# Kernel optimization log

Hardware: AMD Instinct MI355X
Metric: run time of the kernel (lower is better)

## Reference

```python
import jax, jax.numpy as jnp
import numpy as np

D_MODEL = 1024
N_HEADS = 16
D_HEAD = D_MODEL // N_HEADS
ROPE_BASE = 10000.0
EPS = float(jnp.finfo(jnp.float32).eps)  # torch RMSNorm default eps


def _rmsnorm(x, g):
    # x: (..., d_head), g: (d_head,)
    var = jnp.mean(x * x, axis=-1, keepdims=True)
    return x * jax.lax.rsqrt(var + EPS) * g


def _rope(x, pos):
    # x: (B, H, L, d), pos: (L,) int
    d = x.shape[-1]
    inv_freq = 1.0 / (ROPE_BASE ** (jnp.arange(0, d, 2, dtype=jnp.float32) / d))  # (d/2,)
    ang = pos.astype(jnp.float32)[:, None] * inv_freq[None, :]                    # (L, d/2)
    cos, sin = jnp.cos(ang), jnp.sin(ang)                                         # (L, d/2)
    x1, x2 = jnp.split(x, 2, axis=-1)
    return jnp.concatenate([x1 * cos - x2 * sin, x1 * sin + x2 * cos], axis=-1)


def setup_inputs() -> dict:
    key = jax.random.key(0)
    ks = jax.random.split(key, 6)
    B, Lq, Lk = 4, 2048, 2048
    s = 0.02
    return {
        "queries": jax.random.normal(ks[0], (B, Lq, D_MODEL), dtype=jnp.float32),
        "kv": jax.random.normal(ks[1], (B, Lk, D_MODEL), dtype=jnp.float32),
        "Wq": jax.random.normal(ks[2], (D_MODEL, D_MODEL), dtype=jnp.float32) * s,
        "Wkv": jax.random.normal(ks[3], (D_MODEL, 2 * D_MODEL), dtype=jnp.float32) * s,
        "Wout": jax.random.normal(ks[4], (D_MODEL, D_MODEL), dtype=jnp.float32) * s,
        "g_q": jnp.ones((D_HEAD,), dtype=jnp.float32),
        "g_k": jnp.ones((D_HEAD,), dtype=jnp.float32),
        "pos_q": jnp.arange(Lq, dtype=jnp.int64 if jax.config.jax_enable_x64 else jnp.int32),
        "pos_k": jnp.arange(Lk, dtype=jnp.int64 if jax.config.jax_enable_x64 else jnp.int32),
    }


def reference(queries, kv, Wq, Wkv, Wout, g_q, g_k, pos_q, pos_k):
    B, Lq, D = queries.shape
    Lk = kv.shape[1]
    H, d = N_HEADS, D_HEAD
    # projections (bias=False)
    q = (queries @ Wq).reshape(B, Lq, H, d).transpose(0, 2, 1, 3)          # (B,H,Lq,d)
    kvp = (kv @ Wkv).reshape(B, Lk, H, 2 * d).transpose(0, 2, 1, 3)        # (B,H,Lk,2d)
    k, v = kvp[..., :d], kvp[..., d:]
    # per-head RMSNorm on q/k
    q = _rmsnorm(q, g_q)
    k = _rmsnorm(k, g_k)
    # RoPE
    q = _rope(q, pos_q)
    k = _rope(k, pos_k)
    # attention (non-causal, no mask, no dropout)
    scale = d ** -0.5
    scores = jnp.einsum("bhqd,bhkd->bhqk", q, k) * scale                   # (B,H,Lq,Lk)
    attn = jax.nn.softmax(scores, axis=-1)
    y = jnp.einsum("bhqk,bhkd->bhqd", attn, v)                             # (B,H,Lq,d)
    y = y.transpose(0, 2, 1, 3).reshape(B, Lq, D)
    return y @ Wout
```

## Files before the change

kernel.cpp:

```cpp
#include <hip/hip_runtime.h>

#define DEVI __device__ __forceinline__

typedef __bf16 bf16;
typedef __attribute__((ext_vector_type(8))) __bf16 bf16x8v;
typedef __attribute__((ext_vector_type(4))) __bf16 bf16x4v;
typedef __attribute__((ext_vector_type(16))) float f32x16;

constexpr int LKV = 2048;

DEVI void gload16(const void* g, void* l) {
  __builtin_amdgcn_global_load_lds((__attribute__((address_space(1))) void*)g,
                                   (__attribute__((address_space(3))) void*)l, 16, 0, 0);
}

DEVI bf16x8v ldfrag(const bf16* base, int row, int clog) {
  int cphys = clog ^ (row & 7);
  return *(const bf16x8v*)(base + row * 64 + cphys * 8);
}

DEVI unsigned pk2(float a, float b) {
  unsigned short ha = __builtin_bit_cast(unsigned short, (__bf16)a);
  unsigned short hb = __builtin_bit_cast(unsigned short, (__bf16)b);
  return (unsigned)ha | ((unsigned)hb << 16);
}

__global__ void cast_bf16_kernel(const float* __restrict__ in, bf16* __restrict__ out, int n8) {
  int i = blockIdx.x * blockDim.x + threadIdx.x;
  if (i >= n8) return;
  long base = (long)i * 8;
  float4 a = *(const float4*)(in + base);
  float4 b = *(const float4*)(in + base + 4);
  bf16x8v v;
  v[0] = (bf16)a.x; v[1] = (bf16)a.y; v[2] = (bf16)a.z; v[3] = (bf16)a.w;
  v[4] = (bf16)b.x; v[5] = (bf16)b.y; v[6] = (bf16)b.z; v[7] = (bf16)b.w;
  *(bf16x8v*)(out + base) = v;
}

__global__ void wtrans_kernel(const float* __restrict__ W, bf16* __restrict__ Wt, int K, int N) {
  __shared__ float t[32][33];
  int n0 = blockIdx.x * 32, k0 = blockIdx.y * 32;
  int tx = threadIdx.x, ty = threadIdx.y;
  #pragma unroll
  for (int i = 0; i < 4; ++i) t[ty + i * 8][tx] = W[(long)(k0 + ty + i * 8) * N + n0 + tx];
  __syncthreads();
  #pragma unroll
  for (int i = 0; i < 4; ++i) Wt[(long)(n0 + ty + i * 8) * K + k0 + tx] = (bf16)t[tx][ty + i * 8];
}

template<bool OUT_BF16>
__global__ __launch_bounds__(256, 2)
void gemm_bf16_kernel(const bf16* __restrict__ A, const bf16* __restrict__ Bt,
                      void* __restrict__ C, int M, int N, int K, int NXB) {
  __shared__ bf16 As[128 * 64];
  __shared__ bf16 Bs[128 * 64];
  const int tid = threadIdx.x;
  const int wid = tid >> 6, lane = tid & 63;
  const int ln31 = lane & 31, hi = lane >> 5;
  const int wr = wid >> 1, wc = wid & 1;
  const int cpx = gridDim.x >> 3;
  const int wg = blockIdx.x;
  const int flat = (wg & 7) * cpx + (wg >> 3);
  const int by = flat / NXB, bx = flat - by * NXB;
  const int tM = by * 128, tN = bx * 128;
  f32x16 acc[2][2] = {};
  for (int kt = 0; kt < K; kt += 64) {
    #pragma unroll
    for (int p = 0; p < 8; ++p) {
      int cidx = p * 4 + wid;
      int row = (cidx & 15) * 8 + (lane >> 3);
      int clog = (lane & 7) ^ (row & 7);
      if (cidx < 16)
        gload16(A + (long)(tM + row) * K + kt + clog * 8, As + cidx * 512);
      else
        gload16(Bt + (long)(tN + row) * K + kt + clog * 8, Bs + (cidx - 16) * 512);
    }
    __syncthreads();
    #pragma unroll
    for (int st = 0; st < 4; ++st) {
      int clog = st * 2 + hi;
      bf16x8v a0 = ldfrag(As, wr * 64 + ln31, clog);
      bf16x8v a1 = ldfrag(As, wr * 64 + 32 + ln31, clog);
      bf16x8v b0 = ldfrag(Bs, wc * 64 + ln31, clog);
      bf16x8v b1 = ldfrag(Bs, wc * 64 + 32 + ln31, clog);
      acc[0][0] = __builtin_amdgcn_mfma_f32_32x32x16_bf16(a0, b0, acc[0][0], 0, 0, 0);
      acc[0][1] = __builtin_amdgcn_mfma_f32_32x32x16_bf16(a0, b1, acc[0][1], 0, 0, 0);
      acc[1][0] = __builtin_amdgcn_mfma_f32_32x32x16_bf16(a1, b0, acc[1][0], 0, 0, 0);
      acc[1][1] = __builtin_amdgcn_mfma_f32_32x32x16_bf16(a1, b1, acc[1][1], 0, 0, 0);
    }
    __syncthreads();
  }
  #pragma unroll
  for (int mi = 0; mi < 2; ++mi)
    #pragma unroll
    for (int ni = 0; ni < 2; ++ni)
      #pragma unroll
      for (int rr = 0; rr < 4; ++rr)
        #pragma unroll
        for (int j = 0; j < 4; ++j) {
          int mrow = tM + wr * 64 + mi * 32 + rr * 8 + hi * 4 + j;
          int ncol = tN + wc * 64 + ni * 32 + ln31;
          float v = acc[mi][ni][rr * 4 + j];
          if (OUT_BF16) ((bf16*)C)[(long)mrow * N + ncol] = (bf16)v;
          else          ((float*)C)[(long)mrow * N + ncol] = v;
        }
}

__global__ void rope_tab_kernel(const int* __restrict__ pos, float2* __restrict__ tab, float scale) {
  int idx = blockIdx.x * 256 + threadIdx.x;
  int l = idx >> 5, i = idx & 31;
  float ang = (float)pos[l] * __expf((float)i * -0.28782313662425575f);
  float sn, cs;
  sincosf(ang, &sn, &cs);
  tab[idx] = make_float2(cs * scale, sn * scale);
}

__global__ void rope_qk_kernel(const bf16* __restrict__ X, bf16* __restrict__ Out,
                               const float* __restrict__ g, const float2* __restrict__ tab,
                               int colStride, int colOff) {
  int tid = threadIdx.x; int wid = tid >> 6; int lane = tid & 63;
  long w = (long)blockIdx.x * 4 + wid;
  int h = (int)(w & 15); long bl = w >> 4;
  int l = (int)(bl & 2047); int b = (int)(bl >> 11);
  float x = (float)X[bl * colStride + h * colOff + lane];
  float ss = x * x;
  #pragma unroll
  for (int m = 32; m >= 1; m >>= 1) ss += __shfl_xor(ss, m);
  float rs = rsqrtf(ss * (1.0f / 64.0f) + 1.1920928955078125e-07f);
  x *= rs * g[lane];
  float other = __shfl_xor(x, 32);
  float2 cssn = tab[l * 32 + (lane & 31)];
  float y = x * cssn.x + ((lane < 32) ? -other : other) * cssn.y;
  int bh = b * 16 + h;
  Out[((long)bh * 2048 + l) * 64 + lane] = (bf16)y;
}

__global__ void transpose_v_kernel(const unsigned short* __restrict__ KVp, unsigned short* __restrict__ Vt) {
  __shared__ unsigned short t[64][65];
  int bh = blockIdx.y; int b = bh >> 4, h = bh & 15;
  long lt = (long)blockIdx.x * 64;
  int tid = threadIdx.x; int c = tid & 63; int r0 = tid >> 6;
  #pragma unroll
  for (int i = 0; i < 16; ++i) {
    int l = i * 4 + r0;
    t[l][c] = KVp[((long)(b * 2048) + lt + l) * 2048 + h * 128 + 64 + c];
  }
  __syncthreads();
  #pragma unroll
  for (int i = 0; i < 16; ++i) {
    int dv = i * 4 + r0;
    Vt[((long)(bh * 64 + dv)) * 2048 + lt + c] = t[c][dv];
  }
}

__global__ __launch_bounds__(256, 2)
void attn_kernel(const bf16* __restrict__ Q, const bf16* __restrict__ Kr,
                 const bf16* __restrict__ Vt, bf16* __restrict__ Y) {
  __shared__ bf16 Ks[2 * 4096];
  __shared__ bf16 Vs[2 * 4096];
  const int tid = threadIdx.x, wid = tid >> 6, lane = tid & 63;
  const int ln31 = lane & 31, hi = lane >> 5;
  const int wg = blockIdx.x;
  const int flat = (wg & 7) * 128 + (wg >> 3);
  const int bh = flat >> 4, qb = flat & 15;
  const int qg = qb * 128 + wid * 32 + ln31;

  const int rsub = lane >> 3, csub = lane & 7;
  int r0 = wid * 8 + rsub;        int s0 = csub ^ (r0 & 7);
  int r1 = (wid + 4) * 8 + rsub;  int s1 = csub ^ (r1 & 7);
  const bf16* gp0 = Kr + ((long)bh * 2048 + r0) * 64 + s0 * 8;
  const bf16* gp1 = Kr + ((long)bh * 2048 + r1) * 64 + s1 * 8;
  const bf16* gp2 = Vt + ((long)(bh * 64 + r0)) * 2048 + s0 * 8;
  const bf16* gp3 = Vt + ((long)(bh * 64 + r1)) * 2048 + s1 * 8;
  bf16* lk0 = Ks + wid * 512;
  bf16* lk1 = Ks + (wid + 4) * 512;
  bf16* lv0 = Vs + wid * 512;
  bf16* lv1 = Vs + (wid + 4) * 512;

  const bf16* Qrow = Q + ((long)bh * 2048 + qg) * 64;
  bf16x8v qf[4];
  #pragma unroll
  for (int st = 0; st < 4; ++st) qf[st] = *(const bf16x8v*)(Qrow + st * 16 + hi * 8);
  f32x16 o[2] = {};
  float srun = 0.0f;

  gload16(gp0, lk0); gp0 += 4096;
  gload16(gp1, lk1); gp1 += 4096;
  gload16(gp2, lv0); gp2 += 64;
  gload16(gp3, lv1); gp3 += 64;
  __syncthreads();

  int boff = 0;
  for (int kt = 0; kt < LKV; kt += 64) {
    if (kt + 64 < LKV) {
      int nb = boff ^ 4096;
      gload16(gp0, lk0 + nb); gp0 += 4096;
      gload16(gp1, lk1 + nb); gp1 += 4096;
      gload16(gp2, lv0 + nb); gp2 += 64;
      gload16(gp3, lv1 + nb); gp3 += 64;
    }
    const bf16* kb = Ks + boff;
    const bf16* vb = Vs + boff;

    f32x16 sT[2] = {};
    #pragma unroll
    for (int st = 0; st < 4; ++st) {
      int clog = st * 2 + hi;
      bf16x8v k0 = ldfrag(kb, ln31, clog);
      bf16x8v k1 = ldfrag(kb, 32 + ln31, clog);
      sT[0] = __builtin_amdgcn_mfma_f32_32x32x16_bf16(k0, qf[st], sT[0], 0, 0, 0);
      sT[1] = __builtin_amdgcn_mfma_f32_32x32x16_bf16(k1, qf[st], sT[1], 0, 0, 0);
    }

    float p0 = 0.0f, p1 = 0.0f, p2 = 0.0f, p3 = 0.0f;
    #pragma unroll
    for (int mf = 0; mf < 2; ++mf) {
      #pragma unroll
      for (int r = 0; r < 16; r += 4) {
        float e0 = __builtin_amdgcn_exp2f(sT[mf][r + 0]);
        float e1 = __builtin_amdgcn_exp2f(sT[mf][r + 1]);
        float e2 = __builtin_amdgcn_exp2f(sT[mf][r + 2]);
        float e3 = __builtin_amdgcn_exp2f(sT[mf][r + 3]);
        sT[mf][r + 0] = e0; sT[mf][r + 1] = e1; sT[mf][r + 2] = e2; sT[mf][r + 3] = e3;
        p0 += e0; p1 += e1; p2 += e2; p3 += e3;
      }
    }
    srun += (p0 + p1) + (p2 + p3);

    #pragma unroll
    for (int kb_ = 0; kb_ < 4; ++kb_) {
      int mf = kb_ >> 1; int rb = (kb_ & 1) * 8;
      unsigned w0 = pk2(sT[mf][rb + 0], sT[mf][rb + 1]);
      unsigned w1 = pk2(sT[mf][rb + 2], sT[mf][rb + 3]);
      unsigned w2 = pk2(sT[mf][rb + 4], sT[mf][rb + 5]);
      unsigned w3 = pk2(sT[mf][rb + 6], sT[mf][rb + 7]);
      asm("v_permlane32_swap_b32 %0, %1" : "+v"(w0), "+v"(w2));
      asm("v_permlane32_swap_b32 %0, %1" : "+v"(w1), "+v"(w3));
      uint4 uw = make_uint4(w0, w1, w2, w3);
      bf16x8v pf = __builtin_bit_cast(bf16x8v, uw);
      int clog = kb_ * 2 + hi;
      bf16x8v v0 = ldfrag(vb, ln31, clog);
      bf16x8v v1 = ldfrag(vb, 32 + ln31, clog);
      o[0] = __builtin_amdgcn_mfma_f32_32x32x16_bf16(v0, pf, o[0], 0, 0, 0);
      o[1] = __builtin_amdgcn_mfma_f32_32x32x16_bf16(v1, pf, o[1], 0, 0, 0);
    }
    __syncthreads();
    boff ^= 4096;
  }

  srun += __shfl_xor(srun, 32);
  float inv = 1.0f / srun;
  int b = bh >> 4, h = bh & 15;
  long orow = ((long)(b * 2048 + qg)) * 1024 + h * 64;
  #pragma unroll
  for (int mfo = 0; mfo < 2; ++mfo)
    #pragma unroll
    for (int rr = 0; rr < 4; ++rr) {
      bf16x4v wv;
      #pragma unroll
      for (int j = 0; j < 4; ++j) wv[j] = (bf16)(o[mfo][rr * 4 + j] * inv);
      *(bf16x4v*)(Y + orow + mfo * 32 + rr * 8 + hi * 4) = wv;
    }
}

extern "C" void kernel_launch(void* const* d_in, const int* in_sizes, int n_in,
                              void* d_out, int out_size, void* d_ws, size_t ws_size,
                              hipStream_t stream) {
  const float* queries = (const float*)d_in[0];
  const float* kv      = (const float*)d_in[1];
  const float* Wq      = (const float*)d_in[2];
  const float* Wkv     = (const float*)d_in[3];
  const float* Wout    = (const float*)d_in[4];
  const float* g_q     = (const float*)d_in[5];
  const float* g_k     = (const float*)d_in[6];
  const int*   pos_q   = (const int*)d_in[7];
  const int*   pos_k   = (const int*)d_in[8];

  char* ws = (char*)d_ws;
  bf16* Qb    = (bf16*)ws; ws += (long)8192 * 1024 * 2;
  bf16* KVb   = (bf16*)ws; ws += (long)8192 * 1024 * 2;
  bf16* Wqt   = (bf16*)ws; ws += (long)1024 * 1024 * 2;
  bf16* Wkvt  = (bf16*)ws; ws += (long)2048 * 1024 * 2;
  bf16* Woutt = (bf16*)ws; ws += (long)1024 * 1024 * 2;
  bf16* Qp    = (bf16*)ws; ws += (long)8192 * 1024 * 2;
  bf16* KVp   = (bf16*)ws; ws += (long)8192 * 2048 * 2;
  bf16* Qr    = (bf16*)ws; ws += (long)8192 * 1024 * 2;
  bf16* Kr    = (bf16*)ws; ws += (long)8192 * 1024 * 2;
  bf16* Vt    = (bf16*)ws; ws += (long)8192 * 1024 * 2;
  bf16* Y     = (bf16*)ws; ws += (long)8192 * 1024 * 2;
  float2* tabq = (float2*)ws; ws += (long)65536 * 8;
  float2* tabk = (float2*)ws; ws += (long)65536 * 8;

  rope_tab_kernel<<<256, 256, 0, stream>>>(pos_q, tabq, 0.18033688011112042f);
  rope_tab_kernel<<<256, 256, 0, stream>>>(pos_k, tabk, 1.0f);

  cast_bf16_kernel<<<4096, 256, 0, stream>>>(queries, Qb, 8192 * 1024 / 8);
  cast_bf16_kernel<<<4096, 256, 0, stream>>>(kv, KVb, 8192 * 1024 / 8);
  wtrans_kernel<<<dim3(32, 32), dim3(32, 8), 0, stream>>>(Wq, Wqt, 1024, 1024);
  wtrans_kernel<<<dim3(64, 32), dim3(32, 8), 0, stream>>>(Wkv, Wkvt, 1024, 2048);
  wtrans_kernel<<<dim3(32, 32), dim3(32, 8), 0, stream>>>(Wout, Woutt, 1024, 1024);

  gemm_bf16_kernel<true><<<512, 256, 0, stream>>>(Qb, Wqt, Qp, 8192, 1024, 1024, 8);
  gemm_bf16_kernel<true><<<1024, 256, 0, stream>>>(KVb, Wkvt, KVp, 8192, 2048, 1024, 16);

  rope_qk_kernel<<<32768, 256, 0, stream>>>(Qp, Qr, g_q, tabq, 1024, 64);
  rope_qk_kernel<<<32768, 256, 0, stream>>>(KVp, Kr, g_k, tabk, 2048, 128);
  transpose_v_kernel<<<dim3(32, 64), 256, 0, stream>>>((const unsigned short*)KVp, (unsigned short*)Vt);

  attn_kernel<<<1024, 256, 0, stream>>>(Qr, Kr, Vt, Y);

  gemm_bf16_kernel<false><<<512, 256, 0, stream>>>(Y, Woutt, d_out, 8192, 1024, 1024, 8);
}
```

Measured before the change: 367.2 us.

## Replace projection GEMMs with 4-stage LDS ring pipeline and merge small kernels

The projection GEMMs are replaced by a 512-thread kernel with 128x256 or 256x256 tiles and K-step 32. It keeps a 4-deep LDS ring of async global-to-LDS loads (three stages in flight), uses a new swizzle, and raises wave priority around the MFMA block. It also merges the rope-table, cast, weight-transpose and rope kernels into single launches each. The aim is to hide global load latency behind MFMA work, raise tile reuse, and cut launch count. In exchange, LDS use per block is larger and the vmcnt counts are tuned by hand, so wrong counts would break correctness.

```diff
diff --git a/kernel.cpp b/kernel.cpp
--- a/kernel.cpp
+++ b/kernel.cpp
@@ -19,15 +19,24 @@
   return *(const bf16x8v*)(base + row * 64 + cphys * 8);
 }
 
+DEVI bf16x8v ldfrag_r(const bf16* R, int row, int c) {
+  int line = row >> 2;
+  int phys = ((row & 3) * 4 + c) ^ (line & 15);
+  return *(const bf16x8v*)(R + line * 128 + phys * 8);
+}
+
 DEVI unsigned pk2(float a, float b) {
   unsigned short ha = __builtin_bit_cast(unsigned short, (__bf16)a);
   unsigned short hb = __builtin_bit_cast(unsigned short, (__bf16)b);
   return (unsigned)ha | ((unsigned)hb << 16);
 }
 
-__global__ void cast_bf16_kernel(const float* __restrict__ in, bf16* __restrict__ out, int n8) {
-  int i = blockIdx.x * blockDim.x + threadIdx.x;
-  if (i >= n8) return;
+__global__ void cast2_kernel(const float* __restrict__ q, const float* __restrict__ kvp,
+                             bf16* __restrict__ Qb, bf16* __restrict__ KVb) {
+  int i = blockIdx.x * 256 + threadIdx.x;
+  const float* in; bf16* out;
+  if (i < 1048576) { in = q; out = Qb; }
+  else             { in = kvp; out = KVb; i -= 1048576; }
   long base = (long)i * 8;
   float4 a = *(const float4*)(in + base);
   float4 b = *(const float4*)(in + base + 4);
@@ -37,77 +46,116 @@
   *(bf16x8v*)(out + base) = v;
 }
 
-__global__ void wtrans_kernel(const float* __restrict__ W, bf16* __restrict__ Wt, int K, int N) {
+__global__ void wtrans3_kernel(const float* __restrict__ Wq, const float* __restrict__ Wkv,
+                               const float* __restrict__ Wout,
+                               bf16* __restrict__ Wqt, bf16* __restrict__ Wkvt,
+                               bf16* __restrict__ Woutt) {
   __shared__ float t[32][33];
-  int n0 = blockIdx.x * 32, k0 = blockIdx.y * 32;
+  int x = blockIdx.x;
+  const float* W; bf16* Wt; int N; int xb;
+  if (x < 32)      { W = Wq;   Wt = Wqt;   N = 1024; xb = x; }
+  else if (x < 96) { W = Wkv;  Wt = Wkvt;  N = 2048; xb = x - 32; }
+  else             { W = Wout; Wt = Woutt; N = 1024; xb = x - 96; }
+  int n0 = xb * 32, k0 = blockIdx.y * 32;
   int tx = threadIdx.x, ty = threadIdx.y;
   #pragma unroll
   for (int i = 0; i < 4; ++i) t[ty + i * 8][tx] = W[(long)(k0 + ty + i * 8) * N + n0 + tx];
   __syncthreads();
   #pragma unroll
-  for (int i = 0; i < 4; ++i) Wt[(long)(n0 + ty + i * 8) * K + k0 + tx] = (bf16)t[tx][ty + i * 8];
-}
-
-template<bool OUT_BF16>
-__global__ __launch_bounds__(256, 2)
-void gemm_bf16_kernel(const bf16* __restrict__ A, const bf16* __restrict__ Bt,
+  for (int i = 0; i < 4; ++i) Wt[(long)(n0 + ty + i * 8) * 1024 + k0 + tx] = (bf16)t[tx][ty + i * 8];
+}
+
+template<int BM, bool OUT_BF16>
+__global__ __launch_bounds__(512, 2)
+void gemm_ring_kernel(const bf16* __restrict__ A, const bf16* __restrict__ Bt,
                       void* __restrict__ C, int M, int N, int K, int NXB) {
-  __shared__ bf16 As[128 * 64];
-  __shared__ bf16 Bs[128 * 64];
+  constexpr int ROWS = BM + 256;
+  constexpr int REG  = ROWS * 32;
+  constexpr int NCH  = ROWS * 4;
+  constexpr int LPT  = NCH / 512;
+  constexpr int MI   = BM / 64;
+  __shared__ bf16 Lds[4 * REG];
   const int tid = threadIdx.x;
   const int wid = tid >> 6, lane = tid & 63;
   const int ln31 = lane & 31, hi = lane >> 5;
-  const int wr = wid >> 1, wc = wid & 1;
+  const int wm = wid >> 2, wn = wid & 3;
   const int cpx = gridDim.x >> 3;
   const int wg = blockIdx.x;
   const int flat = (wg & 7) * cpx + (wg >> 3);
   const int by = flat / NXB, bx = flat - by * NXB;
-  const int tM = by * 128, tN = bx * 128;
-  f32x16 acc[2][2] = {};
-  for (int kt = 0; kt < K; kt += 64) {
-    #pragma unroll
-    for (int p = 0; p < 8; ++p) {
-      int cidx = p * 4 + wid;
-      int row = (cidx & 15) * 8 + (lane >> 3);
-      int clog = (lane & 7) ^ (row & 7);
-      if (cidx < 16)
-        gload16(A + (long)(tM + row) * K + kt + clog * 8, As + cidx * 512);
-      else
-        gload16(Bt + (long)(tN + row) * K + kt + clog * 8, Bs + (cidx - 16) * 512);
-    }
-    __syncthreads();
-    #pragma unroll
-    for (int st = 0; st < 4; ++st) {
-      int clog = st * 2 + hi;
-      bf16x8v a0 = ldfrag(As, wr * 64 + ln31, clog);
-      bf16x8v a1 = ldfrag(As, wr * 64 + 32 + ln31, clog);
-      bf16x8v b0 = ldfrag(Bs, wc * 64 + ln31, clog);
-      bf16x8v b1 = ldfrag(Bs, wc * 64 + 32 + ln31, clog);
-      acc[0][0] = __builtin_amdgcn_mfma_f32_32x32x16_bf16(a0, b0, acc[0][0], 0, 0, 0);
-      acc[0][1] = __builtin_amdgcn_mfma_f32_32x32x16_bf16(a0, b1, acc[0][1], 0, 0, 0);
-      acc[1][0] = __builtin_amdgcn_mfma_f32_32x32x16_bf16(a1, b0, acc[1][0], 0, 0, 0);
-      acc[1][1] = __builtin_amdgcn_mfma_f32_32x32x16_bf16(a1, b1, acc[1][1], 0, 0, 0);
-    }
-    __syncthreads();
+  const long tM = (long)by * BM, tN = (long)bx * 256;
+  const int NS = K >> 5;
+
+  auto stage = [&](int s) {
+    bf16* region = Lds + (s & 3) * REG;
+    int kcol = s * 32;
+    #pragma unroll
+    for (int q = 0; q < LPT; ++q) {
+      int ci = q * 512 + tid;
+      int line = ci >> 4, phys = ci & 15;
+      int t = phys ^ (line & 15);
+      int row = line * 4 + (t >> 2), c = t & 3;
+      const bf16* src = (row < BM)
+        ? A  + (tM + row) * (long)K + kcol + c * 8
+        : Bt + (tN + row - BM) * (long)K + kcol + c * 8;
+      gload16(src, region + ci * 8);
+    }
+  };
+
+  f32x16 acc[MI][2] = {};
+  stage(0); stage(1); stage(2);
+
+  for (int s = 0; s < NS; ++s) {
+    if constexpr (LPT == 4) asm volatile("s_waitcnt vmcnt(8)" ::: "memory");
+    else                    asm volatile("s_waitcnt vmcnt(6)" ::: "memory");
+    __builtin_amdgcn_s_barrier();
+    __builtin_amdgcn_sched_barrier(0);
+    stage(s + 3);
+    const bf16* R = Lds + (s & 3) * REG;
+    bf16x8v a[MI][2], b[2][2];
+    #pragma unroll
+    for (int mi = 0; mi < MI; ++mi)
+      #pragma unroll
+      for (int ks = 0; ks < 2; ++ks)
+        a[mi][ks] = ldfrag_r(R, wm * (BM / 2) + mi * 32 + ln31, ks * 2 + hi);
+    #pragma unroll
+    for (int ni = 0; ni < 2; ++ni)
+      #pragma unroll
+      for (int ks = 0; ks < 2; ++ks)
+        b[ni][ks] = ldfrag_r(R, BM + wn * 64 + ni * 32 + ln31, ks * 2 + hi);
+    __builtin_amdgcn_s_setprio(1);
+    #pragma unroll
+    for (int ks = 0; ks < 2; ++ks)
+      #pragma unroll
+      for (int mi = 0; mi < MI; ++mi)
+        #pragma unroll
+        for (int ni = 0; ni < 2; ++ni)
+          acc[mi][ni] = __builtin_amdgcn_mfma_f32_32x32x16_bf16(a[mi][ks], b[ni][ks], acc[mi][ni], 0, 0, 0);
+    __builtin_amdgcn_s_setprio(0);
   }
-  #pragma unroll
-  for (int mi = 0; mi < 2; ++mi)
+
+  #pragma unroll
+  for (int mi = 0; mi < MI; ++mi)
     #pragma unroll
     for (int ni = 0; ni < 2; ++ni)
       #pragma unroll
       for (int rr = 0; rr < 4; ++rr)
         #pragma unroll
         for (int j = 0; j < 4; ++j) {
-          int mrow = tM + wr * 64 + mi * 32 + rr * 8 + hi * 4 + j;
-          int ncol = tN + wc * 64 + ni * 32 + ln31;
+          long mrow = tM + wm * (BM / 2) + mi * 32 + rr * 8 + hi * 4 + j;
+          long ncol = tN + wn * 64 + ni * 32 + ln31;
           float v = acc[mi][ni][rr * 4 + j];
-          if (OUT_BF16) ((bf16*)C)[(long)mrow * N + ncol] = (bf16)v;
-          else          ((float*)C)[(long)mrow * N + ncol] = v;
+          if (OUT_BF16) ((bf16*)C)[mrow * N + ncol] = (bf16)v;
+          else          ((float*)C)[mrow * N + ncol] = v;
         }
 }
 
-__global__ void rope_tab_kernel(const int* __restrict__ pos, float2* __restrict__ tab, float scale) {
+__global__ void rope_tab2_kernel(const int* __restrict__ pos_q, const int* __restrict__ pos_k,
+                                 float2* __restrict__ tabq, float2* __restrict__ tabk) {
   int idx = blockIdx.x * 256 + threadIdx.x;
+  const int* pos; float2* tab; float scale;
+  if (idx < 65536) { pos = pos_q; tab = tabq; scale = 0.18033688011112042f; }
+  else             { pos = pos_k; tab = tabk; scale = 1.0f; idx -= 65536; }
   int l = idx >> 5, i = idx & 31;
   float ang = (float)pos[l] * __expf((float)i * -0.28782313662425575f);
   float sn, cs;
@@ -115,11 +163,20 @@
   tab[idx] = make_float2(cs * scale, sn * scale);
 }
 
-__global__ void rope_qk_kernel(const bf16* __restrict__ X, bf16* __restrict__ Out,
-                               const float* __restrict__ g, const float2* __restrict__ tab,
-                               int colStride, int colOff) {
+__global__ void rope2_kernel(const bf16* __restrict__ Qp, const bf16* __restrict__ KVp,
+                             bf16* __restrict__ Qr, bf16* __restrict__ Kr,
+                             const float* __restrict__ g_q, const float* __restrict__ g_k,
+                             const float2* __restrict__ tabq, const float2* __restrict__ tabk) {
+  int bx = blockIdx.x;
+  bool isQ = bx < 32768;
+  int bb = isQ ? bx : bx - 32768;
+  const bf16* X = isQ ? Qp : KVp;
+  bf16* Out = isQ ? Qr : Kr;
+  const float* g = isQ ? g_q : g_k;
+  const float2* tab = isQ ? tabq : tabk;
+  int colStride = isQ ? 1024 : 2048, colOff = isQ ? 64 : 128;
   int tid = threadIdx.x; int wid = tid >> 6; int lane = tid & 63;
-  long w = (long)blockIdx.x * 4 + wid;
+  long w = (long)bb * 4 + wid;
   int h = (int)(w & 15); long bl = w >> 4;
   int l = (int)(bl & 2047); int b = (int)(bl >> 11);
   float x = (float)X[bl * colStride + h * colOff + lane];
@@ -291,23 +348,17 @@
   float2* tabq = (float2*)ws; ws += (long)65536 * 8;
   float2* tabk = (float2*)ws; ws += (long)65536 * 8;
 
-  rope_tab_kernel<<<256, 256, 0, stream>>>(pos_q, tabq, 0.18033688011112042f);
-  rope_tab_kernel<<<256, 256, 0, stream>>>(pos_k, tabk, 1.0f);
-
-  cast_bf16_kernel<<<4096, 256, 0, stream>>>(queries, Qb, 8192 * 1024 / 8);
-  cast_bf16_kernel<<<4096, 256, 0, stream>>>(kv, KVb, 8192 * 1024 / 8);
-  wtrans_kernel<<<dim3(32, 32), dim3(32, 8), 0, stream>>>(Wq, Wqt, 1024, 1024);
-  wtrans_kernel<<<dim3(64, 32), dim3(32, 8), 0, stream>>>(Wkv, Wkvt, 1024, 2048);
-  wtrans_kernel<<<dim3(32, 32), dim3(32, 8), 0, stream>>>(Wout, Woutt, 1024, 1024);
-
-  gemm_bf16_kernel<true><<<512, 256, 0, stream>>>(Qb, Wqt, Qp, 8192, 1024, 1024, 8);
-  gemm_bf16_kernel<true><<<1024, 256, 0, stream>>>(KVb, Wkvt, KVp, 8192, 2048, 1024, 16);
-
-  rope_qk_kernel<<<32768, 256, 0, stream>>>(Qp, Qr, g_q, tabq, 1024, 64);
-  rope_qk_kernel<<<32768, 256, 0, stream>>>(KVp, Kr, g_k, tabk, 2048, 128);
+  rope_tab2_kernel<<<512, 256, 0, stream>>>(pos_q, pos_k, tabq, tabk);
+  cast2_kernel<<<8192, 256, 0, stream>>>(queries, kv, Qb, KVb);
+  wtrans3_kernel<<<dim3(128, 32), dim3(32, 8), 0, stream>>>(Wq, Wkv, Wout, Wqt, Wkvt, Woutt);
+
+  gemm_ring_kernel<128, true><<<256, 512, 0, stream>>>(Qb, Wqt, Qp, 8192, 1024, 1024, 4);
+  gemm_ring_kernel<256, true><<<256, 512, 0, stream>>>(KVb, Wkvt, KVp, 8192, 2048, 1024, 8);
+
+  rope2_kernel<<<65536, 256, 0, stream>>>(Qp, KVp, Qr, Kr, g_q, g_k, tabq, tabk);
   transpose_v_kernel<<<dim3(32, 64), 256, 0, stream>>>((const unsigned short*)KVp, (unsigned short*)Vt);
 
   attn_kernel<<<1024, 256, 0, stream>>>(Qr, Kr, Vt, Y);
 
-  gemm_bf16_kernel<false><<<512, 256, 0, stream>>>(Y, Woutt, d_out, 8192, 1024, 1024, 8);
-}
+  gemm_ring_kernel<128, false><<<256, 512, 0, stream>>>(Y, Woutt, d_out, 8192, 1024, 1024, 4);
+}
```

Result: no change. 365.5 us (-0.5%).
